# Kernel optimization log

Measured on AMD Instinct MI355X. Metric: run time of the kernel, lower is better.

The kernel has to match this reference:

```python
import jax, jax.numpy as jnp
import numpy as np

F_DIM = 256
DFF = 2048      # torch TransformerEncoderLayer default dim_feedforward
NHEAD = 4
NCLS = 7
MAXLEN = 256
BATCH = 256
LN_EPS = 1e-5


def _layer_norm(x, g, b):
    m = x.mean(-1, keepdims=True)
    v = ((x - m) ** 2).mean(-1, keepdims=True)
    return (x - m) / jnp.sqrt(v + LN_EPS) * g + b


def _pos_encoding(n, d):
    # NOTE: original code builds PE over x.size(1) (the batch dim) -- kept faithfully.
    pos = jnp.arange(n, dtype=jnp.float32)[:, None]
    div = jnp.exp(jnp.arange(0, d, 2, dtype=jnp.float32) * (-np.log(10000.0) / d))
    pe = jnp.zeros((n, d), dtype=jnp.float32)
    pe = pe.at[:, 0::2].set(jnp.sin(pos * div))
    pe = pe.at[:, 1::2].set(jnp.cos(pos * div))
    return pe


def _mha(x, Wqkv, bqkv, Wo, bo):
    # x: [S, B, F]  (torch MHA default seq-first layout)
    S, B, F = x.shape
    hd = F // NHEAD
    qkv = x @ Wqkv.T + bqkv                      # [S, B, 3F]
    q, k, v = jnp.split(qkv, 3, axis=-1)
    rs = lambda t: t.reshape(S, B, NHEAD, hd).transpose(1, 2, 0, 3)  # [B, h, S, hd]
    q, k, v = rs(q), rs(k), rs(v)
    attn = jax.nn.softmax(jnp.einsum('bhsd,bhtd->bhst', q, k) / jnp.float32(np.sqrt(hd)), axis=-1)
    o = jnp.einsum('bhst,bhtd->bhsd', attn, v).transpose(2, 0, 1, 3).reshape(S, B, F)
    return o @ Wo.T + bo


def _forward(U_s, U_p, W_emb, b_emb, Wqkv, bqkv, Wo, bo, ln1_g, ln1_b,
             W1, b1, W2, b2, ln2_g, ln2_b, W_fc, b_fc, W_sm, b_sm, seq_lengths):
    L = np.asarray(seq_lengths)                   # static host lengths
    T, B, F = U_s.shape
    mask = jnp.arange(T)[:, None] < jnp.asarray(L)[None, :]        # [T, B] valid-turn mask
    bank_s = U_s * mask[:, :, None]               # zero-padded, as feature_transfer does
    # ---- ReasonMod / MultiTurnTransformer (post-LN encoder layer, eval mode) ----
    h = bank_s @ W_emb.T + b_emb
    h = h + _pos_encoding(B, F)                   # faithful quirk: PE over batch dim
    a_out = _mha(h, Wqkv, bqkv, Wo, bo)
    h1 = _layer_norm(h + a_out, ln1_g, ln1_b)
    ff = jax.nn.relu(h1 @ W1.T + b1) @ W2.T + b2
    h2 = _layer_norm(h1 + ff, ln2_g, ln2_b)
    q = h + h2                                    # [T, B, F]; identical for every t in the loop
    # ---- gather + segment-softmax + scatter-add attention pooling, all t at once ----
    e = jnp.einsum('ibf,tbf->tib', U_p, q)        # scores per (target t, turn i, conv b)
    e = jnp.where(mask[None, :, :], e, -1e30)
    a = jax.nn.softmax(e, axis=1) * mask[None, :, :]
    r = jnp.einsum('tib,ibf->tbf', a, U_p * mask[:, :, None])      # scatter_add equivalent
    rc = jnp.concatenate([bank_s, r], axis=-1)    # [T, B, 2F]
    hidden = jax.nn.relu(rc @ W_fc.T + b_fc)
    logp = jax.nn.log_softmax(hidden @ W_sm.T + b_sm, axis=2)      # [T, B, n_classes]
    rows = np.concatenate([np.arange(l) for l in L])
    cols = np.repeat(np.arange(B), L)
    return logp[rows, cols]                       # [total_tokens, n_classes]


def setup_inputs() -> dict:
    key = jax.random.key(0)
    ks = jax.random.split(key, 24)
    rn = lambda k, shape, s=0.05: jax.random.normal(k, shape, dtype=jnp.float32) * s
    F, D2 = F_DIM, 2 * F_DIM
    inp = {
        'U_s': jax.random.normal(ks[0], (MAXLEN, BATCH, F), dtype=jnp.float32),
        'U_p': jax.random.normal(ks[1], (MAXLEN, BATCH, F), dtype=jnp.float32),
        'W_emb': rn(ks[2], (F, F)), 'b_emb': jnp.zeros((F,), jnp.float32),
        'Wqkv': rn(ks[3], (3 * F, F)), 'bqkv': jnp.zeros((3 * F,), jnp.float32),
        'Wo': rn(ks[4], (F, F)), 'bo': jnp.zeros((F,), jnp.float32),
        'ln1_g': jnp.ones((F,), jnp.float32), 'ln1_b': jnp.zeros((F,), jnp.float32),
        'W1': rn(ks[5], (DFF, F)), 'b1': jnp.zeros((DFF,), jnp.float32),
        'W2': rn(ks[6], (F, DFF)), 'b2': jnp.zeros((F,), jnp.float32),
        'ln2_g': jnp.ones((F,), jnp.float32), 'ln2_b': jnp.zeros((F,), jnp.float32),
        'W_fc': rn(ks[7], (D2, D2)), 'b_fc': jnp.zeros((D2,), jnp.float32),
        'W_sm': rn(ks[8], (NCLS, D2)), 'b_sm': jnp.zeros((NCLS,), jnp.float32),
        'seq_lengths': jax.random.randint(ks[9], (BATCH,), MAXLEN // 2, MAXLEN + 1),
    }
    return inp


def reference(U_s, U_p, W_emb, b_emb, Wqkv, bqkv, Wo, bo, ln1_g, ln1_b,
              W1, b1, W2, b2, ln2_g, ln2_b, W_fc, b_fc, W_sm, b_sm, seq_lengths):
    return _forward(U_s, U_p, W_emb, b_emb, Wqkv, bqkv, Wo, bo, ln1_g, ln1_b,
                    W1, b1, W2, b2, ln2_g, ln2_b, W_fc, b_fc, W_sm, b_sm, seq_lengths)
```

## Files before the change

kernel.cpp:

```cpp
#include <hip/hip_runtime.h>

#define MTB 65536

typedef unsigned int uint;
typedef unsigned short ushort;

typedef _Float16 h8 __attribute__((ext_vector_type(8)));
typedef __attribute__((ext_vector_type(4))) float f4;

enum { E_BIAS=1, E_RELU=2, E_ACC=4, E_RES=8, E_PE=16, E_MASKA=32 };

__device__ __forceinline__ float ldsc(const float* p) { return *p; }
__device__ __forceinline__ float ldsc(const _Float16* p) { return (float)*p; }

template<int EPI, int AMODE, int BMODE, typename CT, int CPL, typename RT, int RPL>
__global__ __launch_bounds__(256) void gemm_h(
    int M, int N, int K,
    const void* __restrict__ Ap, const void* __restrict__ Ap2, int lda, long batchA,
    const void* __restrict__ Bp, int ldw, long batchW,
    CT* __restrict__ C, long cplane, int ldc, long batchC,
    const float* __restrict__ bias,
    const RT* __restrict__ res, const RT* __restrict__ resLo,
    const float* __restrict__ pe,
    const int* __restrict__ seqlen)
{
    __shared__ _Float16 Ah[128][40];
    __shared__ _Float16 Al[(AMODE==3)?128:1][40];
    __shared__ _Float16 Bh[128][40];
    __shared__ _Float16 Bl[(BMODE==0)?128:1][40];

    const int z = blockIdx.z;
    C += (size_t)z * batchC;
    const float*    Af  = (const float*)Ap + (AMODE==0 ? (size_t)z*batchA : 0);
    const _Float16* Ahp = (const _Float16*)Ap + ((AMODE==2||AMODE==3) ? (size_t)z*batchA : 0);
    const _Float16* Alp = (const _Float16*)Ap2 + (AMODE==3 ? (size_t)z*batchA : 0);
    const float*    Bf  = (const float*)Bp + (BMODE!=2 ? (size_t)z*batchW : 0);
    const _Float16* Bhp = (const _Float16*)Bp;

    const int m0 = blockIdx.y * 128, n0 = blockIdx.x * 128;
    const int tid = threadIdx.x;
    const int lane = tid & 63, wid = tid >> 6;
    const int wr = wid >> 1, wc = wid & 1;

    f4 acc[4][4];
    {
        f4 zr = {0.f, 0.f, 0.f, 0.f};
        #pragma unroll
        for (int i = 0; i < 4; i++)
            #pragma unroll
            for (int j = 0; j < 4; j++) acc[i][j] = zr;
    }

    for (int k0 = 0; k0 < K; k0 += 32) {
        __syncthreads();
        if (AMODE == 0 || (AMODE == 4 && k0 < 256)) {
            #pragma unroll
            for (int i = 0; i < 4; i++) {
                const int row = i*32 + (tid>>3);
                const int cg  = (tid&7)<<2;
                const int m = m0 + row;
                float4 v; v.x=0.f; v.y=0.f; v.z=0.f; v.w=0.f;
                bool ok = true;
                if (EPI & E_MASKA) ok = ((m>>8) < seqlen[m&255]);
                if (ok) v = *(const float4*)(Af + (size_t)m*lda + k0 + cg);
                Ah[row][cg+0] = (_Float16)v.x;
                Ah[row][cg+1] = (_Float16)v.y;
                Ah[row][cg+2] = (_Float16)v.z;
                Ah[row][cg+3] = (_Float16)v.w;
            }
        } else if (AMODE == 4) {
            const _Float16* Ar = (const _Float16*)Ap2;
            const int row = tid >> 1;
            const int cg  = (tid & 1) << 4;
            const size_t off = (size_t)(m0 + row) * 256 + (k0 - 256) + cg;
            *(uint4*)&Ah[row][cg]     = *(const uint4*)(Ar + off);
            *(uint4*)&Ah[row][cg + 8] = *(const uint4*)(Ar + off + 8);
        } else {
            const int row = tid >> 1;
            const int cg  = (tid & 1) << 4;
            const size_t off = (size_t)(m0 + row) * lda + k0 + cg;
            *(uint4*)&Ah[row][cg]     = *(const uint4*)(Ahp + off);
            *(uint4*)&Ah[row][cg + 8] = *(const uint4*)(Ahp + off + 8);
            if (AMODE == 3) {
                *(uint4*)&Al[row][cg]     = *(const uint4*)(Alp + off);
                *(uint4*)&Al[row][cg + 8] = *(const uint4*)(Alp + off + 8);
            }
        }
        if (BMODE == 2) {
            const int row = tid >> 1;
            const int cg  = (tid & 1) << 4;
            const size_t off = (size_t)(n0 + row) * ldw + k0 + cg;
            *(uint4*)&Bh[row][cg]     = *(const uint4*)(Bhp + off);
            *(uint4*)&Bh[row][cg + 8] = *(const uint4*)(Bhp + off + 8);
        } else if (BMODE == 0) {
            #pragma unroll
            for (int i = 0; i < 4; i++) {
                const int row = i*32 + (tid>>3);
                const int cg  = (tid&7)<<2;
                float4 v = *(const float4*)(Bf + (size_t)(n0+row)*ldw + k0 + cg);
                _Float16 h0 = (_Float16)v.x, h1 = (_Float16)v.y,
                         h2 = (_Float16)v.z, h3 = (_Float16)v.w;
                Bh[row][cg+0]=h0; Bl[row][cg+0]=(_Float16)(v.x-(float)h0);
                Bh[row][cg+1]=h1; Bl[row][cg+1]=(_Float16)(v.y-(float)h1);
                Bh[row][cg+2]=h2; Bl[row][cg+2]=(_Float16)(v.z-(float)h2);
                Bh[row][cg+3]=h3; Bl[row][cg+3]=(_Float16)(v.w-(float)h3);
            }
        } else {
            #pragma unroll
            for (int i = 0; i < 4; i++) {
                const int kr = i*8 + (tid>>5);
                const int ng = (tid&31)<<2;
                float4 v = *(const float4*)(Bf + (size_t)(k0+kr)*ldw + n0 + ng);
                Bh[ng+0][kr] = (_Float16)v.x;
                Bh[ng+1][kr] = (_Float16)v.y;
                Bh[ng+2][kr] = (_Float16)v.z;
                Bh[ng+3][kr] = (_Float16)v.w;
            }
        }
        __syncthreads();
        const int lr = lane & 15, lk = (lane>>4)<<3;
        h8 ah[4], bh[4];
        #pragma unroll
        for (int i = 0; i < 4; i++) {
            ah[i] = *(const h8*)&Ah[wr*64 + i*16 + lr][lk];
            bh[i] = *(const h8*)&Bh[wc*64 + i*16 + lr][lk];
        }
        #pragma unroll
        for (int mi = 0; mi < 4; mi++)
            #pragma unroll
            for (int ni = 0; ni < 4; ni++)
                acc[mi][ni] = __builtin_amdgcn_mfma_f32_16x16x32_f16(ah[mi], bh[ni], acc[mi][ni], 0, 0, 0);
        if (AMODE == 3) {
            h8 al[4], bl[4];
            #pragma unroll
            for (int i = 0; i < 4; i++) {
                al[i] = *(const h8*)&Al[wr*64 + i*16 + lr][lk];
                bl[i] = *(const h8*)&Bl[wc*64 + i*16 + lr][lk];
            }
            #pragma unroll
            for (int mi = 0; mi < 4; mi++)
                #pragma unroll
                for (int ni = 0; ni < 4; ni++) {
                    acc[mi][ni] = __builtin_amdgcn_mfma_f32_16x16x32_f16(ah[mi], bl[ni], acc[mi][ni], 0, 0, 0);
                    acc[mi][ni] = __builtin_amdgcn_mfma_f32_16x16x32_f16(al[mi], bh[ni], acc[mi][ni], 0, 0, 0);
                }
        }
    }
    const int colb = n0 + wc*64;
    const int rowb = m0 + wr*64;
    #pragma unroll
    for (int ni = 0; ni < 4; ni++) {
        const int col = colb + ni*16 + (lane & 15);
        float bv = (EPI & E_BIAS) ? bias[col] : 0.f;
        #pragma unroll
        for (int mi = 0; mi < 4; mi++) {
            const int r0 = rowb + mi*16 + ((lane>>4)<<2);
            #pragma unroll
            for (int j = 0; j < 4; j++) {
                const int row = r0 + j;
                const size_t idx = (size_t)row*ldc + col;
                float v = acc[mi][ni][j] + bv;
                if (EPI & E_PE)  v += pe[((row & 255) << 8) + col];
                if (EPI & E_RES) {
                    v += ldsc(res + idx);
                    if (RPL) v += ldsc(resLo + idx);
                }
                CT* cp = C + idx;
                if (EPI & E_ACC) v += ldsc((const CT*)cp);
                if (EPI & E_RELU) v = fmaxf(v, 0.f);
                if (CPL) {
                    _Float16 hh = (_Float16)v;
                    *(_Float16*)cp = hh;
                    *((_Float16*)cp + cplane) = (_Float16)(v - (float)hh);
                } else if (sizeof(CT) == 2) {
                    *(_Float16*)cp = (_Float16)v;
                } else {
                    *(float*)cp = v;
                }
            }
        }
    }
}

__global__ __launch_bounds__(256) void ff_kernel(
    const _Float16* __restrict__ h1,
    const _Float16* __restrict__ W1p,
    const _Float16* __restrict__ W2p,
    const float* __restrict__ b1,
    const float* __restrict__ b2,
    float* __restrict__ res2)
{
    __shared__ _Float16 Bs[256][40];
    __shared__ _Float16 zt[64][136];
    const int m0 = blockIdx.x * 64;
    const int tid = threadIdx.x;
    const int lane = tid & 63, wid = tid >> 6;
    const int wr = wid >> 1, wc = wid & 1;
    const int lr = lane & 15, lg = lane >> 4;
    const int lk = lg << 3;
    const int l4 = lg << 2;

    h8 af[2][8];
    #pragma unroll
    for (int mi = 0; mi < 2; mi++)
        #pragma unroll
        for (int ks = 0; ks < 8; ks++)
            af[mi][ks] = *(const h8*)(h1 + (size_t)(m0 + wr*32 + mi*16 + lr) * 256 + ks*32 + lk);

    f4 acc2[2][8];
    {
        f4 zr = {0.f,0.f,0.f,0.f};
        #pragma unroll
        for (int mi = 0; mi < 2; mi++)
            #pragma unroll
            for (int ni = 0; ni < 8; ni++) acc2[mi][ni] = zr;
    }

    for (int c = 0; c < 16; c++) {
        f4 acc1[2][4];
        {
            f4 zr = {0.f,0.f,0.f,0.f};
            #pragma unroll
            for (int mi = 0; mi < 2; mi++)
                #pragma unroll
                for (int ni = 0; ni < 4; ni++) acc1[mi][ni] = zr;
        }
        for (int ks = 0; ks < 8; ks++) {
            __syncthreads();
            {
                const int row = tid >> 1;
                const int h   = tid & 1;
                const int ccs = ((h + (row >> 3)) & 1) << 4;
                const size_t off = (size_t)(c*128 + row) * 256 + ks*32 + (h << 4);
                *(uint4*)&Bs[row][ccs]     = *(const uint4*)(W1p + off);
                *(uint4*)&Bs[row][ccs + 8] = *(const uint4*)(W1p + off + 8);
            }
            __syncthreads();
            #pragma unroll
            for (int ni = 0; ni < 4; ni++) {
                const int row = wc*64 + ni*16 + lr;
                const int col = ((((lg >> 1) + (row >> 3)) & 1) << 4) + ((lg & 1) << 3);
                const h8 b = *(const h8*)&Bs[row][col];
                acc1[0][ni] = __builtin_amdgcn_mfma_f32_16x16x32_f16(af[0][ks], b, acc1[0][ni], 0, 0, 0);
                acc1[1][ni] = __builtin_amdgcn_mfma_f32_16x16x32_f16(af[1][ks], b, acc1[1][ni], 0, 0, 0);
            }
        }
        #pragma unroll
        for (int ni = 0; ni < 4; ni++) {
            const float bv = b1[c*128 + wc*64 + ni*16 + lr];
            #pragma unroll
            for (int mi = 0; mi < 2; mi++)
                #pragma unroll
                for (int j = 0; j < 4; j++) {
                    float v = acc1[mi][ni][j] + bv;
                    v = fmaxf(v, 0.f);
                    zt[wr*32 + mi*16 + l4 + j][wc*64 + ni*16 + lr] = (_Float16)v;
                }
        }
        __syncthreads();
        for (int kk = 0; kk < 4; kk++) {
            if (kk) __syncthreads();
            {
                const size_t off = (size_t)tid * 2048 + c*128 + kk*32;
                #pragma unroll
                for (int j = 0; j < 4; j++) {
                    const int cg = ((j + (tid >> 3)) & 3) << 3;
                    *(uint4*)&Bs[tid][cg] = *(const uint4*)(W2p + off + 8*j);
                }
            }
            __syncthreads();
            h8 a0 = *(const h8*)&zt[wr*32 +      lr][kk*32 + lk];
            h8 a1 = *(const h8*)&zt[wr*32 + 16 + lr][kk*32 + lk];
            #pragma unroll
            for (int ni = 0; ni < 8; ni++) {
                const int row = wc*128 + ni*16 + lr;
                const int col = ((lg + (row >> 3)) & 3) << 3;
                const h8 b = *(const h8*)&Bs[row][col];
                acc2[0][ni] = __builtin_amdgcn_mfma_f32_16x16x32_f16(a0, b, acc2[0][ni], 0, 0, 0);
                acc2[1][ni] = __builtin_amdgcn_mfma_f32_16x16x32_f16(a1, b, acc2[1][ni], 0, 0, 0);
            }
        }
        __syncthreads();
    }
    #pragma unroll
    for (int ni = 0; ni < 8; ni++) {
        const int col = wc*128 + ni*16 + lr;
        const float bv = b2[col];
        #pragma unroll
        for (int mi = 0; mi < 2; mi++) {
            const int rl = wr*32 + mi*16 + l4;
            #pragma unroll
            for (int j = 0; j < 4; j++) {
                const size_t idx = (size_t)(m0 + rl + j) * 256 + col;
                res2[idx] = acc2[mi][ni][j] + bv + (float)h1[idx];
            }
        }
    }
}

__global__ void cvt_kernel(const float* __restrict__ src, int ld, int cshift,
                           _Float16* __restrict__ dst, int total)
{
    const int i = blockIdx.x * 256 + threadIdx.x;
    if (i >= total) return;
    const int r = i >> cshift, c = i & ((1 << cshift) - 1);
    dst[i] = (_Float16)src[(size_t)r * ld + c];
}

__global__ __launch_bounds__(256) void attn_kernel(const _Float16* __restrict__ qkv,
                                                   _Float16* __restrict__ o)
{
    __shared__ _Float16 Kl[64][68];
    __shared__ _Float16 Vt[64][68];
    __shared__ _Float16 Pl[4][64][68];
    const int b = blockIdx.x, head = blockIdx.y;
    const _Float16* base = qkv + (size_t)b * 768 + head * 64;
    const int tid = threadIdx.x;
    const int lane = tid & 63, wid = tid >> 6;
    const int lr = lane & 15, lg = lane >> 4;
    const int lk = lg << 3;
    const int q0 = wid * 64;

    h8 qf[4][2];
    #pragma unroll
    for (int mi = 0; mi < 4; mi++)
        #pragma unroll
        for (int kk = 0; kk < 2; kk++)
            qf[mi][kk] = *(const h8*)(base + (size_t)(q0 + mi*16 + lr) * 196608 + kk*32 + lk);

    f4 oacc[4][4];
    float m_st[4][4], l_st[4][4];
    {
        f4 zr = {0.f,0.f,0.f,0.f};
        #pragma unroll
        for (int mi = 0; mi < 4; mi++)
            #pragma unroll
            for (int di = 0; di < 4; di++) oacc[mi][di] = zr;
        #pragma unroll
        for (int mi = 0; mi < 4; mi++)
            #pragma unroll
            for (int j = 0; j < 4; j++) { m_st[mi][j] = -1e30f; l_st[mi][j] = 0.f; }
    }

    for (int kt = 0; kt < 4; kt++) {
        __syncthreads();
        {
            const int row = tid >> 2, c0 = (tid & 3) << 4;
            const _Float16* rp = base + (size_t)(kt*64 + row) * 196608;
            *(uint4*)&Kl[row][c0]     = *(const uint4*)(rp + 256 + c0);
            *(uint4*)&Kl[row][c0 + 8] = *(const uint4*)(rp + 256 + c0 + 8);
            const h8 v0 = *(const h8*)(rp + 512 + c0);
            const h8 v1 = *(const h8*)(rp + 512 + c0 + 8);
            #pragma unroll
            for (int j = 0; j < 8; j++) {
                Vt[c0 + j][row]     = v0[j];
                Vt[c0 + 8 + j][row] = v1[j];
            }
        }
        __syncthreads();
        f4 sacc[4][4];
        {
            f4 zr = {0.f,0.f,0.f,0.f};
            #pragma unroll
            for (int mi = 0; mi < 4; mi++)
                #pragma unroll
                for (int ni = 0; ni < 4; ni++) sacc[mi][ni] = zr;
        }
        #pragma unroll
        for (int kk = 0; kk < 2; kk++) {
            h8 kf[4];
            #pragma unroll
            for (int ni = 0; ni < 4; ni++)
                kf[ni] = *(const h8*)&Kl[ni*16 + lr][kk*32 + lk];
            #pragma unroll
            for (int mi = 0; mi < 4; mi++)
                #pragma unroll
                for (int ni = 0; ni < 4; ni++)
                    sacc[mi][ni] = __builtin_amdgcn_mfma_f32_16x16x32_f16(qf[mi][kk], kf[ni], sacc[mi][ni], 0, 0, 0);
        }
        #pragma unroll
        for (int mi = 0; mi < 4; mi++)
            #pragma unroll
            for (int ni = 0; ni < 4; ni++)
                #pragma unroll
                for (int j = 0; j < 4; j++) sacc[mi][ni][j] *= 0.125f;
        #pragma unroll
        for (int mi = 0; mi < 4; mi++) {
            #pragma unroll
            for (int j = 0; j < 4; j++) {
                float tm = fmaxf(fmaxf(sacc[mi][0][j], sacc[mi][1][j]),
                                 fmaxf(sacc[mi][2][j], sacc[mi][3][j]));
                tm = fmaxf(tm, __shfl_xor(tm, 1));
                tm = fmaxf(tm, __shfl_xor(tm, 2));
                tm = fmaxf(tm, __shfl_xor(tm, 4));
                tm = fmaxf(tm, __shfl_xor(tm, 8));
                const float mn = fmaxf(m_st[mi][j], tm);
                const float sc = __expf(m_st[mi][j] - mn);
                m_st[mi][j] = mn;
                float ps = 0.f;
                #pragma unroll
                for (int ni = 0; ni < 4; ni++) {
                    const float p = __expf(sacc[mi][ni][j] - mn);
                    sacc[mi][ni][j] = p;
                    ps += p;
                }
                ps += __shfl_xor(ps, 1);
                ps += __shfl_xor(ps, 2);
                ps += __shfl_xor(ps, 4);
                ps += __shfl_xor(ps, 8);
                l_st[mi][j] = l_st[mi][j] * sc + ps;
                #pragma unroll
                for (int di = 0; di < 4; di++) oacc[mi][di][j] *= sc;
            }
        }
        #pragma unroll
        for (int mi = 0; mi < 4; mi++)
            #pragma unroll
            for (int ni = 0; ni < 4; ni++)
                #pragma unroll
                for (int j = 0; j < 4; j++)
                    Pl[wid][mi*16 + (lg<<2) + j][ni*16 + lr] = (_Float16)sacc[mi][ni][j];
        #pragma unroll
        for (int kk = 0; kk < 2; kk++) {
            h8 pf[4], vf[4];
            #pragma unroll
            for (int mi = 0; mi < 4; mi++)
                pf[mi] = *(const h8*)&Pl[wid][mi*16 + lr][kk*32 + lk];
            #pragma unroll
            for (int di = 0; di < 4; di++)
                vf[di] = *(const h8*)&Vt[di*16 + lr][kk*32 + lk];
            #pragma unroll
            for (int mi = 0; mi < 4; mi++)
                #pragma unroll
                for (int di = 0; di < 4; di++)
                    oacc[mi][di] = __builtin_amdgcn_mfma_f32_16x16x32_f16(pf[mi], vf[di], oacc[mi][di], 0, 0, 0);
        }
    }
    _Float16* obase = o + (size_t)b * 256 + head * 64;
    #pragma unroll
    for (int mi = 0; mi < 4; mi++) {
        #pragma unroll
        for (int j = 0; j < 4; j++) {
            const float inv = 1.f / l_st[mi][j];
            const size_t rowoff = (size_t)(q0 + mi*16 + (lg<<2) + j) * 65536;
            #pragma unroll
            for (int di = 0; di < 4; di++)
                obase[rowoff + di*16 + lr] = (_Float16)(oacc[mi][di][j] * inv);
        }
    }
}

template<int OPL, typename OT>
__global__ __launch_bounds__(256) void ln_kernel(const float* __restrict__ x,
    const float* __restrict__ g, const float* __restrict__ bt,
    const _Float16* __restrict__ addin, const _Float16* __restrict__ addinLo,
    OT* __restrict__ out, long oplane, int nrows)
{
    const int gid = blockIdx.x * 256 + threadIdx.x;
    const int row = gid >> 6;
    const int lane = threadIdx.x & 63;
    if (row >= nrows) return;
    const float* xr = x + (size_t)row * 256;
    float4 v = *(const float4*)(xr + (lane<<2));
    float s = v.x + v.y + v.z + v.w;
    #pragma unroll
    for (int off = 32; off > 0; off >>= 1) s += __shfl_xor(s, off, 64);
    const float mean = s * (1.0f/256.0f);
    const float dx = v.x-mean, dy = v.y-mean, dz = v.z-mean, dw = v.w-mean;
    float ss = dx*dx + dy*dy + dz*dz + dw*dw;
    #pragma unroll
    for (int off = 32; off > 0; off >>= 1) ss += __shfl_xor(ss, off, 64);
    const float inv = rsqrtf(ss * (1.0f/256.0f) + 1e-5f);
    const float4 gv = *(const float4*)(g + (lane<<2));
    const float4 bv = *(const float4*)(bt + (lane<<2));
    float ov[4];
    ov[0] = dx*inv*gv.x + bv.x;
    ov[1] = dy*inv*gv.y + bv.y;
    ov[2] = dz*inv*gv.z + bv.z;
    ov[3] = dw*inv*gv.w + bv.w;
    const size_t base = (size_t)row*256 + (lane<<2);
    if (addin) {
        #pragma unroll
        for (int j = 0; j < 4; j++) {
            ov[j] += (float)addin[base+j];
            if (addinLo) ov[j] += (float)addinLo[base+j];
        }
    }
    #pragma unroll
    for (int j = 0; j < 4; j++) {
        if (OPL) {
            _Float16 hh = (_Float16)ov[j];
            ((_Float16*)out)[base+j] = hh;
            ((_Float16*)out)[base+j+oplane] = (_Float16)(ov[j] - (float)hh);
        } else if (sizeof(OT) == 2) {
            ((_Float16*)out)[base+j] = (_Float16)ov[j];
        } else {
            ((float*)out)[base+j] = ov[j];
        }
    }
}

__global__ __launch_bounds__(256) void smax_kernel(float* __restrict__ e,
                                                   const int* __restrict__ seqlen)
{
    const int gid = blockIdx.x * 256 + threadIdx.x;
    const int row = gid >> 6;
    const int lane = threadIdx.x & 63;
    const int L = seqlen[row >> 8];
    float* er = e + (size_t)row * 256;
    float4 v = *(const float4*)(er + (lane<<2));
    const int i0 = lane << 2;
    const float x0 = (i0+0 < L) ? v.x : -1e30f;
    const float x1 = (i0+1 < L) ? v.y : -1e30f;
    const float x2 = (i0+2 < L) ? v.z : -1e30f;
    const float x3 = (i0+3 < L) ? v.w : -1e30f;
    float mx = fmaxf(fmaxf(x0,x1), fmaxf(x2,x3));
    #pragma unroll
    for (int off = 32; off > 0; off >>= 1) mx = fmaxf(mx, __shfl_xor(mx, off, 64));
    const float p0 = (i0+0 < L) ? __expf(x0-mx) : 0.f;
    const float p1 = (i0+1 < L) ? __expf(x1-mx) : 0.f;
    const float p2 = (i0+2 < L) ? __expf(x2-mx) : 0.f;
    const float p3 = (i0+3 < L) ? __expf(x3-mx) : 0.f;
    float s = p0+p1+p2+p3;
    #pragma unroll
    for (int off = 32; off > 0; off >>= 1) s += __shfl_xor(s, off, 64);
    const float inv = 1.f / s;
    v.x = p0*inv; v.y = p1*inv; v.z = p2*inv; v.w = p3*inv;
    *(float4*)(er + (lane<<2)) = v;
}

__global__ __launch_bounds__(256) void head_kernel(const _Float16* __restrict__ hidden,
    const float* __restrict__ Wsm, const float* __restrict__ bsm,
    const int* __restrict__ seqlen, const int* __restrict__ offs,
    float* __restrict__ out)
{
    const int gid = blockIdx.x * 256 + threadIdx.x;
    const int row = gid >> 6;
    const int lane = threadIdx.x & 63;
    if (row >= MTB) return;
    const int t = row >> 8, b = row & 255;
    if (t >= seqlen[b]) return;
    const _Float16* hr = hidden + (size_t)row * 512;
    const h8 hu = *(const h8*)(hr + lane*8);
    float hv[8];
    #pragma unroll
    for (int j = 0; j < 8; j++) hv[j] = (float)hu[j];
    float lg[7];
    #pragma unroll
    for (int c = 0; c < 7; c++) {
        const float* wr = Wsm + c*512 + lane*8;
        const float4 w0 = *(const float4*)wr;
        const float4 w1 = *(const float4*)(wr + 4);
        float acc = hv[0]*w0.x + hv[1]*w0.y + hv[2]*w0.z + hv[3]*w0.w
                  + hv[4]*w1.x + hv[5]*w1.y + hv[6]*w1.z + hv[7]*w1.w;
        #pragma unroll
        for (int off = 32; off > 0; off >>= 1) acc += __shfl_xor(acc, off, 64);
        lg[c] = acc + bsm[c];
    }
    float mx = lg[0];
    #pragma unroll
    for (int c = 1; c < 7; c++) mx = fmaxf(mx, lg[c]);
    float s = 0.f;
    #pragma unroll
    for (int c = 0; c < 7; c++) s += __expf(lg[c] - mx);
    const float lse = mx + logf(s);
    if (lane == 0) {
        float* orow = out + (size_t)(offs[b] + t) * 7;
        #pragma unroll
        for (int c = 0; c < 7; c++) orow[c] = lg[c] - lse;
    }
}

__global__ void pe_kernel(float* __restrict__ pe)
{
    const int idx = blockIdx.x * 256 + threadIdx.x;
    const int b = idx >> 8, f = idx & 255;
    const int j = f >> 1;
    const float div = expf(-9.210340371976184f * (2.0f * j) * (1.0f/256.0f));
    const float arg = (float)b * div;
    pe[idx] = (f & 1) ? cosf(arg) : sinf(arg);
}

__global__ void prefix_kernel(const int* __restrict__ L, int* __restrict__ offs)
{
    if (threadIdx.x == 0) {
        int acc = 0;
        for (int i = 0; i < 256; i++) { offs[i] = acc; acc += L[i]; }
        offs[256] = acc;
    }
}

__global__ void sentinel_kernel(float* __restrict__ out, float v)
{
    if (threadIdx.x == 0) out[0] = v;
}

extern "C" void kernel_launch(void* const* d_in, const int* in_sizes, int n_in,
                              void* d_out, int out_size, void* d_ws, size_t ws_size,
                              hipStream_t stream)
{
    const float* U_s   = (const float*)d_in[0];
    const float* U_p   = (const float*)d_in[1];
    const float* W_emb = (const float*)d_in[2];
    const float* b_emb = (const float*)d_in[3];
    const float* Wqkv  = (const float*)d_in[4];
    const float* bqkv  = (const float*)d_in[5];
    const float* Wo    = (const float*)d_in[6];
    const float* bo    = (const float*)d_in[7];
    const float* ln1_g = (const float*)d_in[8];
    const float* ln1_b = (const float*)d_in[9];
    const float* W1    = (const float*)d_in[10];
    const float* b1    = (const float*)d_in[11];
    const float* W2    = (const float*)d_in[12];
    const float* b2    = (const float*)d_in[13];
    const float* ln2_g = (const float*)d_in[14];
    const float* ln2_b = (const float*)d_in[15];
    const float* W_fc  = (const float*)d_in[16];
    const float* b_fc  = (const float*)d_in[17];
    const float* W_sm  = (const float*)d_in[18];
    const float* b_sm  = (const float*)d_in[19];
    const int*   seqlen= (const int*)d_in[20];
    float* out = (float*)d_out;

    const size_t MiB = 1024*1024;
    const size_t KiB = 1024;
    char* ws = (char*)d_ws;
    if (ws_size < 193*MiB) {
        sentinel_kernel<<<dim3(1), dim3(64), 0, stream>>>(out, -(float)(ws_size / MiB));
        return;
    }
    const long PL = 16*1024*1024;
    _Float16* h_hi = (_Float16*)(ws);
    _Float16* h_lo = (_Float16*)(ws + 32*MiB);
    int*      offs = (int*)(ws + 64*MiB);
    char*     slot = ws + 64*MiB + 8*KiB;
    _Float16* qkv  = (_Float16*)(ws + 65*MiB);
    _Float16* o    = (_Float16*)(ws + 161*MiB);
    float*    res1 = (float*)(ws + 65*MiB);
    float*    res2 = res1;
    _Float16* h1   = (_Float16*)(ws + 161*MiB);
    _Float16* w1p  = (_Float16*)(ws + 129*MiB);
    _Float16* w2p  = (_Float16*)(ws + 130*MiB);
    _Float16* q_hi = (_Float16*)(ws + 129*MiB);
    _Float16* q_lo = (_Float16*)(ws + 161*MiB);
    float*    e    = (float*)(ws + 65*MiB);
    _Float16* r    = (_Float16*)(ws);
    _Float16* hid  = (_Float16*)(ws + 129*MiB);

    prefix_kernel<<<dim3(1), dim3(64), 0, stream>>>(seqlen, offs);

    _Float16* wp  = (_Float16*)slot;
    float*    pe  = (float*)(slot + 512*KiB);

    cvt_kernel<<<dim3(256), 256, 0, stream>>>(W_emb, 256, 8, wp, 65536);
    pe_kernel<<<dim3(256), dim3(256), 0, stream>>>(pe);
    gemm_h<E_BIAS|E_PE|E_MASKA, 0, 2, _Float16, 1, float, 0>
        <<<dim3(2,512,1), 256, 0, stream>>>(
        MTB,256,256, U_s,nullptr,256,0, wp,256,0, h_hi,PL,256,0,
        b_emb, (const float*)nullptr, nullptr, pe, seqlen);

    cvt_kernel<<<dim3(768), 256, 0, stream>>>(Wqkv, 256, 8, wp, 196608);
    gemm_h<E_BIAS, 2, 2, _Float16, 0, float, 0>
        <<<dim3(6,512,1), 256, 0, stream>>>(
        MTB,768,256, h_hi,nullptr,256,0, wp,256,0, qkv,0,768,0,
        bqkv, (const float*)nullptr, nullptr, nullptr, nullptr);

    attn_kernel<<<dim3(256,4), 256, 0, stream>>>(qkv, o);

    cvt_kernel<<<dim3(256), 256, 0, stream>>>(Wo, 256, 8, wp, 65536);
    gemm_h<E_BIAS|E_RES, 2, 2, float, 0, _Float16, 1>
        <<<dim3(2,512,1), 256, 0, stream>>>(
        MTB,256,256, o,nullptr,256,0, wp,256,0, res1,0,256,0,
        bo, h_hi, h_lo, nullptr, nullptr);

    ln_kernel<0, _Float16><<<dim3(MTB/4), 256, 0, stream>>>(
        res1, ln1_g, ln1_b, nullptr, nullptr, h1, 0, MTB);

    cvt_kernel<<<dim3(2048), 256, 0, stream>>>(W1, 256, 8, w1p, 524288);
    cvt_kernel<<<dim3(2048), 256, 0, stream>>>(W2, 2048, 11, w2p, 524288);
    ff_kernel<<<dim3(1024), 256, 0, stream>>>(h1, w1p, w2p, b1, b2, res2);

    ln_kernel<1, _Float16><<<dim3(MTB/4), 256, 0, stream>>>(
        res2, ln2_g, ln2_b, h_hi, h_lo, q_hi, PL, MTB);

    gemm_h<0, 3, 0, float, 0, float, 0>
        <<<dim3(2,2,256), 256, 0, stream>>>(
        256,256,256, q_hi,q_lo,65536,256, U_p,65536,256, e,0,256,65536,
        nullptr, (const float*)nullptr, nullptr, nullptr, nullptr);

    smax_kernel<<<dim3(MTB/4), 256, 0, stream>>>(e, seqlen);

    gemm_h<0, 0, 1, _Float16, 0, float, 0>
        <<<dim3(2,2,256), 256, 0, stream>>>(
        256,256,256, e,nullptr,256,65536, U_p,65536,256, r,0,65536,256,
        nullptr, (const float*)nullptr, nullptr, nullptr, nullptr);

    cvt_kernel<<<dim3(1024), 256, 0, stream>>>(W_fc, 512, 9, wp, 262144);
    gemm_h<E_BIAS|E_RELU|E_MASKA, 4, 2, _Float16, 0, float, 0>
        <<<dim3(4,512,1), 256, 0, stream>>>(
        MTB,512,512, U_s,r,256,0, wp,512,0, hid,0,512,0,
        b_fc, (const float*)nullptr, nullptr, nullptr, seqlen);

    head_kernel<<<dim3(MTB/4), 256, 0, stream>>>(hid, W_sm, b_sm, seqlen, offs, out);
}
```

Baseline: 937.5 us.

## Register-prefetch next weight tile in FF kernel and repad shared memory

The fused feed-forward kernel now loads the next W1/W2 tile from global memory into registers while the MFMA work on the current shared-memory tile runs, so global load latency overlaps compute. The shared tile row stride changes from 40 to 36 halves, and the XOR-style swizzle is dropped in favour of plain padding with 8-byte stores and loads. The trailing barrier at the end of each chunk is removed. This costs extra registers and splits 16-byte LDS accesses into 8-byte ones, which may hurt occupancy and LDS throughput.

```diff
diff --git a/kernel.cpp b/kernel.cpp
--- a/kernel.cpp
+++ b/kernel.cpp
@@ -12,6 +12,8 @@
 
 __device__ __forceinline__ float ldsc(const float* p) { return *p; }
 __device__ __forceinline__ float ldsc(const _Float16* p) { return (float)*p; }
+
+__device__ __forceinline__ h8 uint4_to_h8(uint4 u) { return __builtin_bit_cast(h8, u); }
 
 template<int EPI, int AMODE, int BMODE, typename CT, int CPL, typename RT, int RPL>
 __global__ __launch_bounds__(256) void gemm_h(
@@ -190,7 +192,7 @@
     const float* __restrict__ b2,
     float* __restrict__ res2)
 {
-    __shared__ _Float16 Bs[256][40];
+    __shared__ _Float16 Bs[256][36];
     __shared__ _Float16 zt[64][136];
     const int m0 = blockIdx.x * 64;
     const int tid = threadIdx.x;
@@ -199,6 +201,7 @@
     const int lr = lane & 15, lg = lane >> 4;
     const int lk = lg << 3;
     const int l4 = lg << 2;
+    const int srow = tid >> 1, sh = tid & 1;
 
     h8 af[2][8];
     #pragma unroll
@@ -214,6 +217,13 @@
         for (int mi = 0; mi < 2; mi++)
             #pragma unroll
             for (int ni = 0; ni < 8; ni++) acc2[mi][ni] = zr;
+    }
+
+    uint4 p1a, p1b;
+    uint4 p2[4];
+    {
+        const _Float16* g = W1p + (size_t)srow * 256 + sh*16;
+        p1a = *(const uint4*)g; p1b = *(const uint4*)(g + 8);
     }
 
     for (int c = 0; c < 16; c++) {
@@ -228,19 +238,28 @@
         for (int ks = 0; ks < 8; ks++) {
             __syncthreads();
             {
-                const int row = tid >> 1;
-                const int h   = tid & 1;
-                const int ccs = ((h + (row >> 3)) & 1) << 4;
-                const size_t off = (size_t)(c*128 + row) * 256 + ks*32 + (h << 4);
-                *(uint4*)&Bs[row][ccs]     = *(const uint4*)(W1p + off);
-                *(uint4*)&Bs[row][ccs + 8] = *(const uint4*)(W1p + off + 8);
+                _Float16* d = &Bs[srow][sh*16];
+                uint2 t0; t0.x=p1a.x; t0.y=p1a.y; *(uint2*)(d+0)  = t0;
+                uint2 t1; t1.x=p1a.z; t1.y=p1a.w; *(uint2*)(d+4)  = t1;
+                uint2 t2; t2.x=p1b.x; t2.y=p1b.y; *(uint2*)(d+8)  = t2;
+                uint2 t3; t3.x=p1b.z; t3.y=p1b.w; *(uint2*)(d+12) = t3;
             }
             __syncthreads();
+            if (ks < 7) {
+                const _Float16* g = W1p + (size_t)(c*128 + srow) * 256 + (ks+1)*32 + sh*16;
+                p1a = *(const uint4*)g; p1b = *(const uint4*)(g + 8);
+            } else {
+                const _Float16* g = W2p + (size_t)tid * 2048 + c*128;
+                #pragma unroll
+                for (int q = 0; q < 4; q++) p2[q] = *(const uint4*)(g + 8*q);
+            }
             #pragma unroll
             for (int ni = 0; ni < 4; ni++) {
-                const int row = wc*64 + ni*16 + lr;
-                const int col = ((((lg >> 1) + (row >> 3)) & 1) << 4) + ((lg & 1) << 3);
-                const h8 b = *(const h8*)&Bs[row][col];
+                const _Float16* s = &Bs[wc*64 + ni*16 + lr][lk];
+                uint2 q0 = *(const uint2*)s;
+                uint2 q1 = *(const uint2*)(s + 4);
+                uint4 u; u.x=q0.x; u.y=q0.y; u.z=q1.x; u.w=q1.y;
+                const h8 b = uint4_to_h8(u);
                 acc1[0][ni] = __builtin_amdgcn_mfma_f32_16x16x32_f16(af[0][ks], b, acc1[0][ni], 0, 0, 0);
                 acc1[1][ni] = __builtin_amdgcn_mfma_f32_16x16x32_f16(af[1][ks], b, acc1[1][ni], 0, 0, 0);
             }
@@ -261,26 +280,35 @@
         for (int kk = 0; kk < 4; kk++) {
             if (kk) __syncthreads();
             {
-                const size_t off = (size_t)tid * 2048 + c*128 + kk*32;
-                #pragma unroll
-                for (int j = 0; j < 4; j++) {
-                    const int cg = ((j + (tid >> 3)) & 3) << 3;
-                    *(uint4*)&Bs[tid][cg] = *(const uint4*)(W2p + off + 8*j);
+                _Float16* d = &Bs[tid][0];
+                #pragma unroll
+                for (int q = 0; q < 4; q++) {
+                    uint2 ta; ta.x=p2[q].x; ta.y=p2[q].y; *(uint2*)(d + 8*q)     = ta;
+                    uint2 tb; tb.x=p2[q].z; tb.y=p2[q].w; *(uint2*)(d + 8*q + 4) = tb;
                 }
             }
             __syncthreads();
-            h8 a0 = *(const h8*)&zt[wr*32 +      lr][kk*32 + lk];
-            h8 a1 = *(const h8*)&zt[wr*32 + 16 + lr][kk*32 + lk];
+            if (kk < 3) {
+                const _Float16* g = W2p + (size_t)tid * 2048 + c*128 + (kk+1)*32;
+                #pragma unroll
+                for (int q = 0; q < 4; q++) p2[q] = *(const uint4*)(g + 8*q);
+            } else if (c < 15) {
+                const _Float16* g = W1p + (size_t)((c+1)*128 + srow) * 256 + sh*16;
+                p1a = *(const uint4*)g; p1b = *(const uint4*)(g + 8);
+            }
+            const h8 a0 = *(const h8*)&zt[wr*32 +      lr][kk*32 + lk];
+            const h8 a1 = *(const h8*)&zt[wr*32 + 16 + lr][kk*32 + lk];
             #pragma unroll
             for (int ni = 0; ni < 8; ni++) {
-                const int row = wc*128 + ni*16 + lr;
-                const int col = ((lg + (row >> 3)) & 3) << 3;
-                const h8 b = *(const h8*)&Bs[row][col];
+                const _Float16* s = &Bs[wc*128 + ni*16 + lr][lk];
+                uint2 q0 = *(const uint2*)s;
+                uint2 q1 = *(const uint2*)(s + 4);
+                uint4 u; u.x=q0.x; u.y=q0.y; u.z=q1.x; u.w=q1.y;
+                const h8 b = uint4_to_h8(u);
                 acc2[0][ni] = __builtin_amdgcn_mfma_f32_16x16x32_f16(a0, b, acc2[0][ni], 0, 0, 0);
                 acc2[1][ni] = __builtin_amdgcn_mfma_f32_16x16x32_f16(a1, b, acc2[1][ni], 0, 0, 0);
             }
         }
-        __syncthreads();
     }
     #pragma unroll
     for (int ni = 0; ni < 8; ni++) {
```

New measurement: 923.3 us. About the same (-1.5%).

## Prefetch FF weight tiles into registers and cut sync count

Applied to the files above, without the earlier changes.

Restructures the fused feed-forward kernel to process 64-column chunks of the hidden dimension (32 chunks instead of 16). It stages whole W1 and W2 chunk tiles through one shared buffer, with the next tile loaded into registers while the current chunk computes. This removes the per-k-step barriers and global loads inside the inner loops, hiding global memory latency. The cost is more register pressure from the prefetch buffers and a different LDS padding layout that may bring bank conflicts.

```diff
diff --git a/kernel.cpp b/kernel.cpp
--- a/kernel.cpp
+++ b/kernel.cpp
@@ -12,6 +12,8 @@
 
 __device__ __forceinline__ float ldsc(const float* p) { return *p; }
 __device__ __forceinline__ float ldsc(const _Float16* p) { return (float)*p; }
+
+__device__ __forceinline__ h8 uint4_to_h8(uint4 u) { return __builtin_bit_cast(h8, u); }
 
 template<int EPI, int AMODE, int BMODE, typename CT, int CPL, typename RT, int RPL>
 __global__ __launch_bounds__(256) void gemm_h(
@@ -190,7 +192,7 @@
     const float* __restrict__ b2,
     float* __restrict__ res2)
 {
-    __shared__ _Float16 Bs[256][40];
+    __shared__ _Float16 WB[17408];
     __shared__ _Float16 zt[64][136];
     const int m0 = blockIdx.x * 64;
     const int tid = threadIdx.x;
@@ -199,6 +201,8 @@
     const int lr = lane & 15, lg = lane >> 4;
     const int lk = lg << 3;
     const int l4 = lg << 2;
+    const int prow = tid >> 2;
+    const int pcol = (tid & 3) << 6;
 
     h8 af[2][8];
     #pragma unroll
@@ -216,71 +220,82 @@
             for (int ni = 0; ni < 8; ni++) acc2[mi][ni] = zr;
     }
 
-    for (int c = 0; c < 16; c++) {
-        f4 acc1[2][4];
+    uint4 pf1[8], pf2[8];
+    {
+        const _Float16* g = W1p + (size_t)prow * 256 + pcol;
+        #pragma unroll
+        for (int q = 0; q < 8; q++) pf1[q] = *(const uint4*)(g + 8*q);
+    }
+
+    for (int c = 0; c < 32; c++) {
+        __syncthreads();
+        {
+            _Float16* d = &WB[prow*264 + pcol];
+            #pragma unroll
+            for (int q = 0; q < 8; q++) *(uint4*)(d + 8*q) = pf1[q];
+        }
+        __syncthreads();
+        {
+            const _Float16* g = W2p + (size_t)tid * 2048 + c*64;
+            #pragma unroll
+            for (int q = 0; q < 8; q++) pf2[q] = *(const uint4*)(g + 8*q);
+        }
+        f4 acc1[2][2];
         {
             f4 zr = {0.f,0.f,0.f,0.f};
-            #pragma unroll
-            for (int mi = 0; mi < 2; mi++)
-                #pragma unroll
-                for (int ni = 0; ni < 4; ni++) acc1[mi][ni] = zr;
-        }
+            acc1[0][0]=zr; acc1[0][1]=zr; acc1[1][0]=zr; acc1[1][1]=zr;
+        }
+        #pragma unroll
         for (int ks = 0; ks < 8; ks++) {
-            __syncthreads();
-            {
-                const int row = tid >> 1;
-                const int h   = tid & 1;
-                const int ccs = ((h + (row >> 3)) & 1) << 4;
-                const size_t off = (size_t)(c*128 + row) * 256 + ks*32 + (h << 4);
-                *(uint4*)&Bs[row][ccs]     = *(const uint4*)(W1p + off);
-                *(uint4*)&Bs[row][ccs + 8] = *(const uint4*)(W1p + off + 8);
-            }
-            __syncthreads();
-            #pragma unroll
-            for (int ni = 0; ni < 4; ni++) {
-                const int row = wc*64 + ni*16 + lr;
-                const int col = ((((lg >> 1) + (row >> 3)) & 1) << 4) + ((lg & 1) << 3);
-                const h8 b = *(const h8*)&Bs[row][col];
-                acc1[0][ni] = __builtin_amdgcn_mfma_f32_16x16x32_f16(af[0][ks], b, acc1[0][ni], 0, 0, 0);
-                acc1[1][ni] = __builtin_amdgcn_mfma_f32_16x16x32_f16(af[1][ks], b, acc1[1][ni], 0, 0, 0);
-            }
-        }
-        #pragma unroll
-        for (int ni = 0; ni < 4; ni++) {
-            const float bv = b1[c*128 + wc*64 + ni*16 + lr];
+            const h8 b0 = *(const h8*)&WB[(wc*32 +      lr)*264 + ks*32 + lk];
+            const h8 b1f = *(const h8*)&WB[(wc*32 + 16 + lr)*264 + ks*32 + lk];
+            acc1[0][0] = __builtin_amdgcn_mfma_f32_16x16x32_f16(af[0][ks], b0,  acc1[0][0], 0, 0, 0);
+            acc1[1][0] = __builtin_amdgcn_mfma_f32_16x16x32_f16(af[1][ks], b0,  acc1[1][0], 0, 0, 0);
+            acc1[0][1] = __builtin_amdgcn_mfma_f32_16x16x32_f16(af[0][ks], b1f, acc1[0][1], 0, 0, 0);
+            acc1[1][1] = __builtin_amdgcn_mfma_f32_16x16x32_f16(af[1][ks], b1f, acc1[1][1], 0, 0, 0);
+        }
+        #pragma unroll
+        for (int ni = 0; ni < 2; ni++) {
+            const float bv = b1[c*64 + wc*32 + ni*16 + lr];
             #pragma unroll
             for (int mi = 0; mi < 2; mi++)
                 #pragma unroll
                 for (int j = 0; j < 4; j++) {
                     float v = acc1[mi][ni][j] + bv;
                     v = fmaxf(v, 0.f);
-                    zt[wr*32 + mi*16 + l4 + j][wc*64 + ni*16 + lr] = (_Float16)v;
+                    zt[wr*32 + mi*16 + l4 + j][wc*32 + ni*16 + lr] = (_Float16)v;
                 }
         }
         __syncthreads();
-        for (int kk = 0; kk < 4; kk++) {
-            if (kk) __syncthreads();
-            {
-                const size_t off = (size_t)tid * 2048 + c*128 + kk*32;
-                #pragma unroll
-                for (int j = 0; j < 4; j++) {
-                    const int cg = ((j + (tid >> 3)) & 3) << 3;
-                    *(uint4*)&Bs[tid][cg] = *(const uint4*)(W2p + off + 8*j);
-                }
-            }
-            __syncthreads();
-            h8 a0 = *(const h8*)&zt[wr*32 +      lr][kk*32 + lk];
-            h8 a1 = *(const h8*)&zt[wr*32 + 16 + lr][kk*32 + lk];
+        {
+            _Float16* d = &WB[tid*68];
+            #pragma unroll
+            for (int q = 0; q < 8; q++) {
+                uint2 ta; ta.x = pf2[q].x; ta.y = pf2[q].y; *(uint2*)(d + 8*q)     = ta;
+                uint2 tb; tb.x = pf2[q].z; tb.y = pf2[q].w; *(uint2*)(d + 8*q + 4) = tb;
+            }
+        }
+        __syncthreads();
+        if (c < 31) {
+            const _Float16* g = W1p + (size_t)((c+1)*64 + prow) * 256 + pcol;
+            #pragma unroll
+            for (int q = 0; q < 8; q++) pf1[q] = *(const uint4*)(g + 8*q);
+        }
+        #pragma unroll
+        for (int kk = 0; kk < 2; kk++) {
+            const h8 a0 = *(const h8*)&zt[wr*32 +      lr][kk*32 + lk];
+            const h8 a1 = *(const h8*)&zt[wr*32 + 16 + lr][kk*32 + lk];
             #pragma unroll
             for (int ni = 0; ni < 8; ni++) {
-                const int row = wc*128 + ni*16 + lr;
-                const int col = ((lg + (row >> 3)) & 3) << 3;
-                const h8 b = *(const h8*)&Bs[row][col];
+                const _Float16* s = &WB[(wc*128 + ni*16 + lr)*68 + kk*32 + lk];
+                uint2 q0 = *(const uint2*)s;
+                uint2 q1 = *(const uint2*)(s + 4);
+                uint4 u; u.x=q0.x; u.y=q0.y; u.z=q1.x; u.w=q1.y;
+                const h8 b = uint4_to_h8(u);
                 acc2[0][ni] = __builtin_amdgcn_mfma_f32_16x16x32_f16(a0, b, acc2[0][ni], 0, 0, 0);
                 acc2[1][ni] = __builtin_amdgcn_mfma_f32_16x16x32_f16(a1, b, acc2[1][ni], 0, 0, 0);
             }
         }
-        __syncthreads();
     }
     #pragma unroll
     for (int ni = 0; ni < 8; ni++) {
```

New measurement: 1.247 ms. +33.1%, slower.
